# Optimization experiments

Hardware: AMD Instinct MI355X
Metric: run time of the kernel (lower is better)

The kernel has to match this reference:

```python
import jax, jax.numpy as jnp
import numpy as np

DIM = 1024
H = 8            # heads (light and heavy)
DH = 64          # dim_head
W = 64           # local attention window (light_window_size // 2)
NQ = 512         # num_heavy_tokens_q
NKV = 1024       # num_heavy_tokens_kv
EPS = 1.0        # coor descent eps
NITERS = 50      # coor descent iters
FETCH = 9.0 / 8.0
SCALE = DH ** -0.5


def _ln(x, w, b):
    m = x.mean(-1, keepdims=True)
    v = ((x - m) ** 2).mean(-1, keepdims=True)
    return (x - m) * jax.lax.rsqrt(v + 1e-5) * w + b


def _rms(x, g):
    n = jnp.maximum(jnp.linalg.norm(x, axis=-1, keepdims=True), 1e-12)
    return x / n * np.sqrt(DIM).astype(np.float32) * g


def local_attn(x, Wqkv, Wout):
    # LocalMHA, non-causal, look_backward=1, look_forward=1, window W
    b, n, _ = x.shape
    nw = n // W
    qkv = x @ Wqkv.T                      # [b,n,3*H*DH]
    q, k, v = jnp.split(qkv, 3, axis=-1)
    def towin(t):
        return t.reshape(b, nw, W, H, DH).transpose(0, 3, 1, 2, 4)  # [b,h,nw,w,dh]
    q, k, v = map(towin, (q, k, v))
    def expand(t):  # gather prev/cur/next windows -> [b,h,nw,3w,dh]
        tp = jnp.pad(t, ((0, 0), (0, 0), (1, 1), (0, 0), (0, 0)))
        return jnp.concatenate([tp[:, :, :-2], tp[:, :, 1:-1], tp[:, :, 2:]], axis=3)
    ke, ve = expand(k), expand(v)
    sim = jnp.einsum('bhnid,bhnjd->bhnij', q, ke) * SCALE
    win = jnp.arange(nw)
    valid = jnp.concatenate([
        jnp.repeat((win > 0)[:, None], W, 1),
        jnp.ones((nw, W), bool),
        jnp.repeat((win < nw - 1)[:, None], W, 1)], axis=1)  # [nw,3w]
    sim = jnp.where(valid[None, None, :, None, :], sim, -1e9)
    attn = jax.nn.softmax(sim, axis=-1)
    o = jnp.einsum('bhnij,bhnjd->bhnid', attn, ve)
    o = o.transpose(0, 2, 3, 1, 4).reshape(b, n, H * DH)
    return o @ Wout.T


def route(x, routing_token, num_tokens):
    # CoordinateDescentRouter with num_routing_tokens=1, straight_through=True
    s = jnp.einsum('bnd,rd->brn', x, routing_token).reshape(x.shape[0], x.shape[1])
    n = s.shape[-1]
    logk = jnp.log(jnp.asarray(min(num_tokens * FETCH, float(n)), s.dtype))
    def body(ab, _):
        a, bb = ab
        a = EPS * (logk - jax.nn.logsumexp((s + bb) / EPS, axis=-1, keepdims=True))
        bb = -jax.nn.relu(s + a)
        return (a, bb), None
    (a, bb), _ = jax.lax.scan(body, (jnp.zeros((s.shape[0], 1), s.dtype), -s), None, length=NITERS)
    scores = jnp.exp((s + a + bb) / EPS)
    sel_scores, sel_idx = jax.lax.top_k(scores, num_tokens)
    # straight-through: forward value 1.0, gradient of identity
    sel_scores = sel_scores + jax.lax.stop_gradient(1.0 - sel_scores)
    return sel_scores, sel_idx


def heavy_attn(xq, ctx, scores_kv, gamma, Wq, Wkv, Wout, null_kv):
    b = xq.shape[0]
    xq = _rms(xq, gamma)
    ctx = _rms(ctx, gamma)
    q = (xq @ Wq.T).reshape(b, -1, H, DH).transpose(0, 2, 1, 3)           # [b,h,nq,dh]
    kv = (ctx @ Wkv.T).reshape(b, -1, H, 2 * DH).transpose(0, 2, 1, 3)    # [b,h,nkv,2dh]
    k, v = kv[..., :DH], kv[..., DH:]
    v = v * scores_kv[:, None, :, None]
    nk = jnp.broadcast_to(null_kv[0][None, :, None, :], (b, H, 1, DH))
    nv = jnp.broadcast_to(null_kv[1][None, :, None, :], (b, H, 1, DH))
    k = jnp.concatenate([nk, k], axis=2)
    v = jnp.concatenate([nv, v], axis=2)
    sim = jnp.einsum('bhid,bhjd->bhij', q, k) * SCALE
    attn = jax.nn.softmax(sim, axis=-1)
    o = jnp.einsum('bhij,bhjd->bhid', attn, v)
    o = o.transpose(0, 2, 1, 3).reshape(b, -1, H * DH)
    return o @ Wout.T


def setup_inputs() -> dict:
    key = jax.random.key(0)
    ks = jax.random.split(key, 12)
    D, IN = DIM, H * DH
    w = lambda k, shape: jax.random.normal(k, shape, jnp.float32) * 0.02
    return {
        'x': jax.random.normal(ks[0], (4, 4096, D), jnp.float32),
        'ln_w': jnp.ones((D,), jnp.float32),
        'ln_b': jnp.zeros((D,), jnp.float32),
        'Wqkv': w(ks[1], (3 * IN, D)),
        'Wout_l': w(ks[2], (D, IN)),
        'rt_q': jax.random.normal(ks[3], (1, D), jnp.float32),
        'rt_kv': jax.random.normal(ks[4], (1, D), jnp.float32),
        'gamma': jnp.ones((D,), jnp.float32),
        'Wq': w(ks[5], (IN, D)),
        'Wkv': w(ks[6], (2 * IN, D)),
        'Wout_h': w(ks[7], (D, IN)),
        'null_kv': jax.random.normal(ks[8], (2, H, DH), jnp.float32),
        'null_q': jax.random.normal(ks[9], (D,), jnp.float32),
    }


def reference(x, ln_w, ln_b, Wqkv, Wout_l, rt_q, rt_kv, gamma, Wq, Wkv, Wout_h, null_kv, null_q):
    b, n, d = x.shape
    light = local_attn(_ln(x, ln_w, ln_b), Wqkv, Wout_l)
    sq, iq = route(x, rt_q, NQ)
    skv, ikv = route(x, rt_kv, NKV)
    br = jnp.arange(b)[:, None]
    xq = x[br, iq]          # gather routed queries  [b,NQ,d]
    xkv = x[br, ikv]        # gather routed kv       [b,NKV,d]
    heavy = heavy_attn(xq, xkv, skv, gamma, Wq, Wkv, Wout_h, null_kv)
    heavy = heavy * sq[..., None]
    out = jnp.broadcast_to(null_q[None, None, :], (b, n, d))
    out = out.at[br, iq].set(heavy)   # scatter heavy branch back
    return out + light
```

## Files before the change

### kernel.cpp

```cpp
#include <hip/hip_runtime.h>
#include <hip/hip_bf16.h>

typedef __attribute__((ext_vector_type(8))) short bv8;
typedef __attribute__((ext_vector_type(4))) float fv4;
typedef __hip_bfloat16 bf16;

#define MFMA16(a,b,c) __builtin_amdgcn_mfma_f32_16x16x32_bf16((a),(b),(c),0,0,0)
#define GLOAD_LDS(gp, lp) __builtin_amdgcn_global_load_lds( \
    (const __attribute__((address_space(1))) void*)(gp), \
    (__attribute__((address_space(3))) void*)(lp), 16, 0, 0)

template<int NW>
__device__ __forceinline__ float blockReduceSumF(float v) {
  #pragma unroll
  for (int m = 1; m < 64; m <<= 1) v += __shfl_xor(v, m, 64);
  __shared__ float sm[NW];
  if ((threadIdx.x & 63) == 0) sm[threadIdx.x >> 6] = v;
  __syncthreads();
  float t = 0.f;
  #pragma unroll
  for (int i = 0; i < NW; ++i) t += sm[i];
  __syncthreads();
  return t;
}

template<int NW>
__device__ __forceinline__ double blockReduceMaxD(double v) {
  #pragma unroll
  for (int m = 1; m < 64; m <<= 1) v = fmax(v, __shfl_xor(v, m, 64));
  __shared__ double sm[NW];
  if ((threadIdx.x & 63) == 0) sm[threadIdx.x >> 6] = v;
  __syncthreads();
  double t = sm[0];
  #pragma unroll
  for (int i = 1; i < NW; ++i) t = fmax(t, sm[i]);
  __syncthreads();
  return t;
}

__global__ __launch_bounds__(256)
void prep_kernel(const float* __restrict__ x, const float* __restrict__ lnw,
                 const float* __restrict__ lnb, const float* __restrict__ rtq,
                 const float* __restrict__ rtkv, bf16* __restrict__ lnout,
                 double* __restrict__ s,
                 const float* __restrict__ a0, const float* __restrict__ a1,
                 const float* __restrict__ a2, const float* __restrict__ a3,
                 const float* __restrict__ a4,
                 bf16* __restrict__ b0, bf16* __restrict__ b1, bf16* __restrict__ b2,
                 bf16* __restrict__ b3, bf16* __restrict__ b4,
                 int* __restrict__ posq) {
  const int bid = blockIdx.x;
  if (bid < 16384) {
    const int r = bid;
    const float* xr = x + (size_t)r * 1024;
    float v4[4]; float ssum = 0.f;
    double dq = 0.0, dk = 0.0;
    #pragma unroll
    for (int i = 0; i < 4; ++i) {
      int d = threadIdx.x + i * 256;
      float v = xr[d];
      v4[i] = v; ssum += v;
      dq += (double)v * (double)rtq[d];
      dk += (double)v * (double)rtkv[d];
    }
    ssum = blockReduceSumF<4>(ssum);
    const float mean = ssum * (1.0f / 1024.0f);
    float vs = 0.f;
    #pragma unroll
    for (int i = 0; i < 4; ++i) { float d = v4[i] - mean; vs += d * d; }
    vs = blockReduceSumF<4>(vs);
    const float rstd = 1.0f / sqrtf(vs * (1.0f / 1024.0f) + 1e-5f);
    #pragma unroll
    for (int m = 1; m < 64; m <<= 1) { dq += __shfl_xor(dq, m, 64); dk += __shfl_xor(dk, m, 64); }
    __shared__ double smq[4], smk[4];
    if ((threadIdx.x & 63) == 0) { smq[threadIdx.x >> 6] = dq; smk[threadIdx.x >> 6] = dk; }
    __syncthreads();
    if (threadIdx.x == 0) {
      s[r] = smq[0] + smq[1] + smq[2] + smq[3];
      s[16384 + r] = smk[0] + smk[1] + smk[2] + smk[3];
    }
    bf16* orow = lnout + (size_t)r * 1024;
    #pragma unroll
    for (int i = 0; i < 4; ++i) {
      int d = threadIdx.x + i * 256;
      orow[d] = __float2bfloat16((v4[i] - mean) * rstd * lnw[d] + lnb[d]);
    }
  } else if (bid < 18432) {
    size_t g = ((size_t)(bid - 16384) * 256 + threadIdx.x) * 8;
    const float* src; bf16* dst; size_t off;
    if (g < 1572864)      { src = a0; dst = b0; off = g; }
    else if (g < 2097152) { src = a1; dst = b1; off = g - 1572864; }
    else if (g < 2621440) { src = a2; dst = b2; off = g - 2097152; }
    else if (g < 3670016) { src = a3; dst = b3; off = g - 2621440; }
    else                  { src = a4; dst = b4; off = g - 3670016; }
    float4 v0 = *(const float4*)(src + off);
    float4 v1 = *(const float4*)(src + off + 4);
    bv8 o;
    ((bf16*)&o)[0] = __float2bfloat16(v0.x); ((bf16*)&o)[1] = __float2bfloat16(v0.y);
    ((bf16*)&o)[2] = __float2bfloat16(v0.z); ((bf16*)&o)[3] = __float2bfloat16(v0.w);
    ((bf16*)&o)[4] = __float2bfloat16(v1.x); ((bf16*)&o)[5] = __float2bfloat16(v1.y);
    ((bf16*)&o)[6] = __float2bfloat16(v1.z); ((bf16*)&o)[7] = __float2bfloat16(v1.w);
    *(bv8*)(dst + off) = o;
  } else {
    int i0 = (bid - 18432) * 1024 + threadIdx.x * 4;
    posq[i0] = -1; posq[i0 + 1] = -1; posq[i0 + 2] = -1; posq[i0 + 3] = -1;
  }
}

__global__ __launch_bounds__(256, 1)
void route_sel_kernel(const double* __restrict__ s_all, int* __restrict__ iq,
                      int* __restrict__ ikv, int* __restrict__ posq) {
  const int route = blockIdx.x >> 2, b = blockIdx.x & 3;
  const double* s = s_all + route * 16384 + b * 4096;
  const double K = (route == 0) ? 576.0 : 1152.0;
  const int KSEL = (route == 0) ? 512 : 1024;
  const int tid = threadIdx.x;
  const int lane = tid & 63, wid = tid >> 6;
  __shared__ double evbuf[4096];
  __shared__ double a_sh;
  __shared__ int scn[256];

  double sv[16];
  #pragma unroll
  for (int i = 0; i < 16; ++i) sv[i] = s[tid * 16 + i];
  double mx = sv[0];
  #pragma unroll
  for (int i = 1; i < 16; ++i) mx = fmax(mx, sv[i]);
  mx = blockReduceMaxD<4>(mx);
  #pragma unroll
  for (int i = 0; i < 16; ++i) evbuf[tid * 16 + i] = exp(sv[i] - mx);
  __syncthreads();

  if (wid == 0) {
    double e64[64];
    #pragma unroll
    for (int j = 0; j < 64; ++j) e64[j] = evbuf[j * 64 + lane];
    double z = (4096.0 / K) * exp(-mx);
    for (int it = 1; it < 50; ++it) {
      double a0 = 0.0, a1 = 0.0, a2 = 0.0, a3 = 0.0;
      #pragma unroll
      for (int j = 0; j < 64; j += 4) {
        a0 += fmin(e64[j], z);
        a1 += fmin(e64[j + 1], z);
        a2 += fmin(e64[j + 2], z);
        a3 += fmin(e64[j + 3], z);
      }
      double t = (a0 + a1) + (a2 + a3);
      #pragma unroll
      for (int m = 1; m < 64; m <<= 1) t += __shfl_xor(t, m, 64);
      z = t / K;
    }
    if (lane == 0) a_sh = -mx - log(z);
  }
  __syncthreads();
  const double a = a_sh;

  float scf[16]; int m16 = 0;
  #pragma unroll
  for (int i = 0; i < 16; ++i) {
    scf[i] = (float)exp(fmin(sv[i] + a, 0.0));
    m16 += (scf[i] == 1.0f) ? 1 : 0;
  }
  scn[tid] = m16;
  __syncthreads();
  for (int off = 1; off < 256; off <<= 1) {
    int v = (tid >= off) ? scn[tid - off] : 0;
    __syncthreads();
    scn[tid] += v;
    __syncthreads();
  }
  const int total = scn[255];
  const int excl = scn[tid] - m16;
  if (total >= KSEL) {
    int rk = excl;
    #pragma unroll
    for (int i = 0; i < 16; ++i) {
      if (scf[i] == 1.0f) {
        if (rk < KSEL) {
          int idx = tid * 16 + i;
          if (route == 0) { iq[b * 512 + rk] = idx; posq[b * 4096 + idx] = rk; }
          else            { ikv[b * 1024 + rk] = idx; }
        }
        rk++;
      }
    }
  } else {
    unsigned long long* keys = (unsigned long long*)evbuf;
    #pragma unroll
    for (int i = 0; i < 16; ++i) {
      unsigned bits = __float_as_uint(scf[i]);
      keys[tid * 16 + i] = ((unsigned long long)(~bits) << 32) | (unsigned long long)(tid * 16 + i);
    }
    for (int k = 2; k <= 4096; k <<= 1) {
      for (int j = k >> 1; j > 0; j >>= 1) {
        __syncthreads();
        for (int t = tid; t < 2048; t += 256) {
          int i2 = ((t & ~(j - 1)) << 1) | (t & (j - 1));
          int ip = i2 + j;
          unsigned long long av = keys[i2], bvv = keys[ip];
          bool up = ((i2 & k) == 0);
          if (up ? (av > bvv) : (av < bvv)) { keys[i2] = bvv; keys[ip] = av; }
        }
      }
    }
    __syncthreads();
    for (int j2 = tid; j2 < KSEL; j2 += 256) {
      int idx = (int)(keys[j2] & 0xFFFFFFFFull);
      if (route == 0) { iq[b * 512 + j2] = idx; posq[b * 4096 + idx] = j2; }
      else            { ikv[b * 1024 + j2] = idx; }
    }
  }
}

template<int EPI>
__device__ __forceinline__ void gemm_core(
    const bf16* __restrict__ A, const bf16* __restrict__ B, void* __restrict__ Cout,
    int N, int K, int row0, int col0, bf16* As, bf16* Bs,
    const int* __restrict__ posq, const float* __restrict__ heavy,
    const float* __restrict__ nullq) {
  const int tid = threadIdx.x;
  const int lane = tid & 63, w = tid >> 6;
  const int wr = w >> 1, wc = w & 1;
  const int lrow = lane & 15, lk = (lane >> 4) * 8;
  fv4 acc[4][4];
  #pragma unroll
  for (int m = 0; m < 4; ++m)
    #pragma unroll
    for (int n = 0; n < 4; ++n) acc[m][n] = (fv4){0.f, 0.f, 0.f, 0.f};
  const int ob0 = w * 2048;
  for (int k0 = 0; k0 < K; k0 += 32) {
    #pragma unroll
    for (int t = 0; t < 2; ++t) {
      int ob = ob0 + t * 1024;
      int ofl = ob + lane * 16;
      int r = ofl >> 6, c8 = ((ofl >> 4) & 3) * 8;
      GLOAD_LDS(A + (size_t)(row0 + r) * K + k0 + c8, (char*)As + ob);
      GLOAD_LDS(B + (size_t)(col0 + r) * K + k0 + c8, (char*)Bs + ob);
    }
    __syncthreads();
    bv8 af[4], bfr[4];
    #pragma unroll
    for (int m = 0; m < 4; ++m) af[m] = *(bv8*)&As[(wr * 64 + m * 16 + lrow) * 32 + lk];
    #pragma unroll
    for (int n = 0; n < 4; ++n) bfr[n] = *(bv8*)&Bs[(wc * 64 + n * 16 + lrow) * 32 + lk];
    #pragma unroll
    for (int m = 0; m < 4; ++m)
      #pragma unroll
      for (int n = 0; n < 4; ++n)
        acc[m][n] = MFMA16(af[m], bfr[n], acc[m][n]);
    __syncthreads();
  }
  #pragma unroll
  for (int m = 0; m < 4; ++m) {
    int gr0 = row0 + wr * 64 + m * 16 + (lane >> 4) * 4;
    #pragma unroll
    for (int n = 0; n < 4; ++n) {
      int gc = col0 + wc * 64 + n * 16 + lrow;
      #pragma unroll
      for (int r = 0; r < 4; ++r) {
        int grow = gr0 + r;
        float vv = acc[m][n][r];
        if (EPI == 0) {
          ((bf16*)Cout)[(size_t)grow * N + gc] = __float2bfloat16(vv);
        } else if (EPI == 1) {
          ((float*)Cout)[(size_t)grow * N + gc] = vv;
        } else {
          int p = posq[grow];
          float add = (p >= 0) ? heavy[((size_t)((grow >> 12) * 512 + p)) * 1024 + gc]
                               : nullq[gc];
          ((float*)Cout)[(size_t)grow * N + gc] = vv + add;
        }
      }
    }
  }
}

__device__ __forceinline__ void xcd_remap(int d, int gx, int& row0, int& col0) {
  int q = d >> 3;
  col0 = (q % gx) * 128;
  row0 = ((d & 7) + 8 * (q / gx)) * 128;
}

template<int EPI>
__global__ __launch_bounds__(256)
void gemm_bt(const bf16* __restrict__ A, const bf16* __restrict__ B, void* __restrict__ Cout,
             int N, int K,
             const int* __restrict__ posq, const float* __restrict__ heavy,
             const float* __restrict__ nullq) {
  __shared__ alignas(16) bf16 As[128 * 32];
  __shared__ alignas(16) bf16 Bs[128 * 32];
  int row0, col0;
  xcd_remap(blockIdx.y * gridDim.x + blockIdx.x, gridDim.x, row0, col0);
  gemm_core<EPI>(A, B, Cout, N, K, row0, col0, As, Bs, posq, heavy, nullq);
}

__global__ __launch_bounds__(256)
void wqkv_gemm_kernel(const bf16* __restrict__ xkv, const bf16* __restrict__ Wkv,
                      bf16* __restrict__ kvh,
                      const bf16* __restrict__ xq, const bf16* __restrict__ Wq,
                      bf16* __restrict__ qh) {
  __shared__ alignas(16) bf16 As[128 * 32];
  __shared__ alignas(16) bf16 Bs[128 * 32];
  const int bid = blockIdx.x;
  int row0, col0;
  if (bid < 256) {
    xcd_remap(bid, 8, row0, col0);
    gemm_core<0>(xkv, Wkv, kvh, 1024, 1024, row0, col0, As, Bs, nullptr, nullptr, nullptr);
  } else {
    xcd_remap(bid - 256, 4, row0, col0);
    gemm_core<0>(xq, Wq, qh, 512, 1024, row0, col0, As, Bs, nullptr, nullptr, nullptr);
  }
}

__global__ __launch_bounds__(256)
void la_gather_kernel(const bf16* __restrict__ qkv, bf16* __restrict__ olight,
                      const float* __restrict__ x, const float* __restrict__ gamma,
                      const int* __restrict__ iq, const int* __restrict__ ikv,
                      bf16* __restrict__ xq, bf16* __restrict__ xkv) {
  __shared__ bf16 Qs[64][72], Ks[64][72], Vts[64][72], Ps[64][72];
  const int tid = threadIdx.x;
  if (blockIdx.x < 2048) {
    const int w = blockIdx.x & 63, h = (blockIdx.x >> 6) & 7, b = blockIdx.x >> 9;
    const int lane = tid & 63, wv = tid >> 6;
    const int lrow = lane & 15, lkg = lane >> 4;
    {
      const size_t baseq = ((size_t)(b * 4096 + w * 64)) * 1536 + h * 64;
      #pragma unroll
      for (int v = 0; v < 2; ++v) {
        int vec = tid + v * 256; int i = vec >> 3, dd = (vec & 7) * 8;
        *(bv8*)&Qs[i][dd] = *(const bv8*)&qkv[baseq + (size_t)i * 1536 + dd];
      }
    }
    fv4 oacc[4];
    float m_run[4], l_run[4];
    #pragma unroll
    for (int n = 0; n < 4; ++n) oacc[n] = (fv4){0.f, 0.f, 0.f, 0.f};
    #pragma unroll
    for (int r = 0; r < 4; ++r) { m_run[r] = -INFINITY; l_run[r] = 0.f; }
    for (int c = 0; c < 3; ++c) {
      int sw = w - 1 + c;
      if (sw < 0 || sw >= 64) continue;
      __syncthreads();
      const size_t bkv = ((size_t)(b * 4096 + sw * 64)) * 1536 + h * 64;
      #pragma unroll
      for (int v = 0; v < 2; ++v) {
        int vec = tid + v * 256; int i = vec >> 3, dd = (vec & 7) * 8;
        *(bv8*)&Ks[i][dd] = *(const bv8*)&qkv[bkv + 512 + (size_t)i * 1536 + dd];
      }
      #pragma unroll
      for (int v = 0; v < 2; ++v) {
        int vec = tid + v * 256; int j = vec >> 3, d0 = (vec & 7) * 8;
        bv8 val = *(const bv8*)&qkv[bkv + 1024 + (size_t)j * 1536 + d0];
        #pragma unroll
        for (int i = 0; i < 8; ++i) Vts[d0 + i][j] = ((bf16*)&val)[i];
      }
      __syncthreads();
      fv4 sa[4];
      #pragma unroll
      for (int n = 0; n < 4; ++n) {
        sa[n] = (fv4){0.f, 0.f, 0.f, 0.f};
        #pragma unroll
        for (int ks = 0; ks < 2; ++ks) {
          bv8 aq = *(bv8*)&Qs[wv * 16 + lrow][lkg * 8 + ks * 32];
          bv8 bk = *(bv8*)&Ks[n * 16 + lrow][lkg * 8 + ks * 32];
          sa[n] = MFMA16(aq, bk, sa[n]);
        }
      }
      float mc[4];
      #pragma unroll
      for (int r = 0; r < 4; ++r) {
        #pragma unroll
        for (int n = 0; n < 4; ++n) sa[n][r] *= 0.125f;
        mc[r] = fmaxf(fmaxf(sa[0][r], sa[1][r]), fmaxf(sa[2][r], sa[3][r]));
      }
      #pragma unroll
      for (int m = 1; m < 16; m <<= 1)
        #pragma unroll
        for (int r = 0; r < 4; ++r) mc[r] = fmaxf(mc[r], __shfl_xor(mc[r], m, 64));
      float p[4][4], ls[4];
      #pragma unroll
      for (int r = 0; r < 4; ++r) {
        float mn = fmaxf(m_run[r], mc[r]);
        float scl = expf(m_run[r] - mn);
        ls[r] = 0.f;
        #pragma unroll
        for (int n = 0; n < 4; ++n) { p[n][r] = expf(sa[n][r] - mn); ls[r] += p[n][r]; }
        m_run[r] = mn;
        l_run[r] *= scl;
        #pragma unroll
        for (int n = 0; n < 4; ++n) oacc[n][r] *= scl;
      }
      #pragma unroll
      for (int m = 1; m < 16; m <<= 1)
        #pragma unroll
        for (int r = 0; r < 4; ++r) ls[r] += __shfl_xor(ls[r], m, 64);
      #pragma unroll
      for (int r = 0; r < 4; ++r) l_run[r] += ls[r];
      #pragma unroll
      for (int n = 0; n < 4; ++n)
        #pragma unroll
        for (int r = 0; r < 4; ++r)
          Ps[wv * 16 + lkg * 4 + r][n * 16 + lrow] = __float2bfloat16(p[n][r]);
      __syncthreads();
      #pragma unroll
      for (int n = 0; n < 4; ++n)
        #pragma unroll
        for (int ks = 0; ks < 2; ++ks) {
          bv8 ap = *(bv8*)&Ps[wv * 16 + lrow][lkg * 8 + ks * 32];
          bv8 bvv = *(bv8*)&Vts[n * 16 + lrow][lkg * 8 + ks * 32];
          oacc[n] = MFMA16(ap, bvv, oacc[n]);
        }
    }
    const size_t ob = ((size_t)(b * 4096 + w * 64 + wv * 16)) * 512 + h * 64;
    #pragma unroll
    for (int n = 0; n < 4; ++n)
      #pragma unroll
      for (int r = 0; r < 4; ++r) {
        int row = lkg * 4 + r;
        olight[ob + (size_t)row * 512 + n * 16 + lrow] = __float2bfloat16(oacc[n][r] / l_run[r]);
      }
  } else {
    const int bid = blockIdx.x - 2048;
    const float* src; bf16* dst;
    if (bid < 2048) {
      int b = bid >> 9, j = bid & 511;
      int tok = iq[b * 512 + j];
      src = x + ((size_t)(b * 4096 + tok)) * 1024;
      dst = xq + (size_t)bid * 1024;
    } else {
      int id = bid - 2048;
      int b = id >> 10, j = id & 1023;
      int tok = ikv[b * 1024 + j];
      src = x + ((size_t)(b * 4096 + tok)) * 1024;
      dst = xkv + (size_t)id * 1024;
    }
    float v4[4]; float ss = 0.f;
    #pragma unroll
    for (int i = 0; i < 4; ++i) { v4[i] = src[tid + i * 256]; ss += v4[i] * v4[i]; }
    ss = blockReduceSumF<4>(ss);
    const float nrm = fmaxf(sqrtf(ss), 1e-12f);
    const float scl = 32.0f / nrm;
    #pragma unroll
    for (int i = 0; i < 4; ++i) {
      int d = tid + i * 256;
      dst[d] = __float2bfloat16(v4[i] * scl * gamma[d]);
    }
  }
}

__global__ __launch_bounds__(256)
void heavy_attn_split_kernel(const bf16* __restrict__ qh, const bf16* __restrict__ kvh,
                             const float* __restrict__ nkv, bf16* __restrict__ o_part,
                             float* __restrict__ ml_part) {
  const int qt = blockIdx.x, h = blockIdx.y;
  const int b = blockIdx.z >> 2, s = blockIdx.z & 3;
  const int tid = threadIdx.x;
  const int lane = tid & 63, wv = tid >> 6;
  const int lrow = lane & 15, lkg = lane >> 4;
  __shared__ bf16 Qs[64][72], Ks[64][72], Vts[64][72], Ps[64][72];
  {
    const size_t baseq = ((size_t)(b * 512 + qt * 64)) * 512 + h * 64;
    #pragma unroll
    for (int v = 0; v < 2; ++v) {
      int vec = tid + v * 256; int i = vec >> 3, dd = (vec & 7) * 8;
      *(bv8*)&Qs[i][dd] = *(const bv8*)&qh[baseq + (size_t)i * 512 + dd];
    }
  }
  fv4 oacc[4];
  float m_run[4], l_run[4];
  #pragma unroll
  for (int n = 0; n < 4; ++n) oacc[n] = (fv4){0.f, 0.f, 0.f, 0.f};
  #pragma unroll
  for (int r = 0; r < 4; ++r) { m_run[r] = -INFINITY; l_run[r] = 0.f; }
  const int cs = (s == 0) ? 0 : (s * 4 + 1);
  const int ce = s * 4 + 5;
  for (int c = cs; c < ce; ++c) {
    __syncthreads();
    #pragma unroll
    for (int v = 0; v < 2; ++v) {
      int vec = tid + v * 256; int j = vec >> 3, dd = (vec & 7) * 8;
      int kvg = c * 64 + j;
      bv8 val;
      if (kvg >= 1 && kvg <= 1024) {
        val = *(const bv8*)&kvh[((size_t)(b * 1024 + kvg - 1)) * 1024 + h * 128 + dd];
      } else if (kvg == 0) {
        #pragma unroll
        for (int t = 0; t < 8; ++t) ((bf16*)&val)[t] = __float2bfloat16(nkv[h * 64 + dd + t]);
      } else {
        #pragma unroll
        for (int t = 0; t < 8; ++t) ((short*)&val)[t] = 0;
      }
      *(bv8*)&Ks[j][dd] = val;
    }
    #pragma unroll
    for (int v = 0; v < 2; ++v) {
      int vec = tid + v * 256; int j = vec >> 3, d0 = (vec & 7) * 8;
      int kvg = c * 64 + j;
      if (kvg >= 1 && kvg <= 1024) {
        bv8 val = *(const bv8*)&kvh[((size_t)(b * 1024 + kvg - 1)) * 1024 + h * 128 + 64 + d0];
        #pragma unroll
        for (int i = 0; i < 8; ++i) Vts[d0 + i][j] = ((bf16*)&val)[i];
      } else if (kvg == 0) {
        #pragma unroll
        for (int i = 0; i < 8; ++i) Vts[d0 + i][j] = __float2bfloat16(nkv[512 + h * 64 + d0 + i]);
      } else {
        #pragma unroll
        for (int i = 0; i < 8; ++i) Vts[d0 + i][j] = __float2bfloat16(0.0f);
      }
    }
    __syncthreads();
    fv4 sa[4];
    #pragma unroll
    for (int n = 0; n < 4; ++n) {
      sa[n] = (fv4){0.f, 0.f, 0.f, 0.f};
      #pragma unroll
      for (int ks = 0; ks < 2; ++ks) {
        bv8 aq = *(bv8*)&Qs[wv * 16 + lrow][lkg * 8 + ks * 32];
        bv8 bk = *(bv8*)&Ks[n * 16 + lrow][lkg * 8 + ks * 32];
        sa[n] = MFMA16(aq, bk, sa[n]);
      }
    }
    float mc[4];
    #pragma unroll
    for (int r = 0; r < 4; ++r) {
      #pragma unroll
      for (int n = 0; n < 4; ++n) {
        sa[n][r] *= 0.125f;
        int kvg = c * 64 + n * 16 + lrow;
        if (kvg > 1024) sa[n][r] = -1e30f;
      }
      mc[r] = fmaxf(fmaxf(sa[0][r], sa[1][r]), fmaxf(sa[2][r], sa[3][r]));
    }
    #pragma unroll
    for (int m = 1; m < 16; m <<= 1)
      #pragma unroll
      for (int r = 0; r < 4; ++r) mc[r] = fmaxf(mc[r], __shfl_xor(mc[r], m, 64));
    float p[4][4], ls[4];
    #pragma unroll
    for (int r = 0; r < 4; ++r) {
      float mn = fmaxf(m_run[r], mc[r]);
      float scl = expf(m_run[r] - mn);
      ls[r] = 0.f;
      #pragma unroll
      for (int n = 0; n < 4; ++n) { p[n][r] = expf(sa[n][r] - mn); ls[r] += p[n][r]; }
      m_run[r] = mn;
      l_run[r] *= scl;
      #pragma unroll
      for (int n = 0; n < 4; ++n) oacc[n][r] *= scl;
    }
    #pragma unroll
    for (int m = 1; m < 16; m <<= 1)
      #pragma unroll
      for (int r = 0; r < 4; ++r) ls[r] += __shfl_xor(ls[r], m, 64);
    #pragma unroll
    for (int r = 0; r < 4; ++r) l_run[r] += ls[r];
    #pragma unroll
    for (int n = 0; n < 4; ++n)
      #pragma unroll
      for (int r = 0; r < 4; ++r)
        Ps[wv * 16 + lkg * 4 + r][n * 16 + lrow] = __float2bfloat16(p[n][r]);
    __syncthreads();
    #pragma unroll
    for (int n = 0; n < 4; ++n)
      #pragma unroll
      for (int ks = 0; ks < 2; ++ks) {
        bv8 ap = *(bv8*)&Ps[wv * 16 + lrow][lkg * 8 + ks * 32];
        bv8 bvv = *(bv8*)&Vts[n * 16 + lrow][lkg * 8 + ks * 32];
        oacc[n] = MFMA16(ap, bvv, oacc[n]);
      }
  }
  const int idx = (((s * 4 + b) * 8 + h) * 8 + qt);
  bf16* ob = o_part + (size_t)idx * 4096;
  #pragma unroll
  for (int n = 0; n < 4; ++n)
    #pragma unroll
    for (int r = 0; r < 4; ++r) {
      int row = wv * 16 + lkg * 4 + r;
      ob[row * 64 + n * 16 + lrow] = __float2bfloat16(oacc[n][r]);
    }
  if (lrow == 0) {
    #pragma unroll
    for (int r = 0; r < 4; ++r) {
      int row = wv * 16 + lkg * 4 + r;
      ml_part[idx * 128 + row] = m_run[r];
      ml_part[idx * 128 + 64 + row] = l_run[r];
    }
  }
}

__global__ __launch_bounds__(256)
void heavy_combine_kernel(const bf16* __restrict__ o_part, const float* __restrict__ ml_part,
                          bf16* __restrict__ oh) {
  const int qt = blockIdx.x, h = blockIdx.y, b = blockIdx.z;
  const int tid = threadIdx.x;
  const int row = tid >> 2, c0 = (tid & 3) * 16;
  int idx[4]; float m[4], l[4];
  #pragma unroll
  for (int s = 0; s < 4; ++s) {
    idx[s] = (((s * 4 + b) * 8 + h) * 8 + qt);
    m[s] = ml_part[idx[s] * 128 + row];
    l[s] = ml_part[idx[s] * 128 + 64 + row];
  }
  const float mstar = fmaxf(fmaxf(m[0], m[1]), fmaxf(m[2], m[3]));
  float wsum = 0.f, w[4];
  #pragma unroll
  for (int s = 0; s < 4; ++s) { w[s] = expf(m[s] - mstar); wsum += w[s] * l[s]; }
  const float inv = 1.0f / wsum;
  float o[16];
  #pragma unroll
  for (int i = 0; i < 16; ++i) o[i] = 0.f;
  #pragma unroll
  for (int s = 0; s < 4; ++s) {
    const bf16* op = o_part + (size_t)idx[s] * 4096 + row * 64 + c0;
    bv8 v0 = *(const bv8*)op;
    bv8 v1 = *(const bv8*)(op + 8);
    #pragma unroll
    for (int j = 0; j < 8; ++j) o[j] += w[s] * __bfloat162float(((bf16*)&v0)[j]);
    #pragma unroll
    for (int j = 0; j < 8; ++j) o[8 + j] += w[s] * __bfloat162float(((bf16*)&v1)[j]);
  }
  const size_t ob = ((size_t)(b * 512 + qt * 64 + row)) * 512 + h * 64 + c0;
  bv8 pk[2];
  #pragma unroll
  for (int i = 0; i < 16; ++i) ((bf16*)pk)[i] = __float2bfloat16(o[i] * inv);
  *(bv8*)&oh[ob] = pk[0];
  *(bv8*)&oh[ob + 8] = pk[1];
}

extern "C" void kernel_launch(void* const* d_in, const int* in_sizes, int n_in,
                              void* d_out, int out_size, void* d_ws, size_t ws_size,
                              hipStream_t stream) {
  (void)in_sizes; (void)n_in; (void)out_size; (void)ws_size;
  const float* x     = (const float*)d_in[0];
  const float* ln_w  = (const float*)d_in[1];
  const float* ln_b  = (const float*)d_in[2];
  const float* Wqkv  = (const float*)d_in[3];
  const float* Woutl = (const float*)d_in[4];
  const float* rtq   = (const float*)d_in[5];
  const float* rtkv  = (const float*)d_in[6];
  const float* gamma = (const float*)d_in[7];
  const float* Wq    = (const float*)d_in[8];
  const float* Wkv   = (const float*)d_in[9];
  const float* Wouth = (const float*)d_in[10];
  const float* nkv   = (const float*)d_in[11];
  const float* nq    = (const float*)d_in[12];
  float* out = (float*)d_out;

  char* ws = (char*)d_ws;
  size_t off = 0;
  auto alloc = [&](size_t bytes) -> void* {
    void* p = ws + off;
    off = (off + bytes + 255) & ~(size_t)255;
    return p;
  };
  bf16* ln_bf    = (bf16*)alloc(16384ull * 1024 * 2);
  bf16* qkv_bf   = (bf16*)alloc(16384ull * 1536 * 2);
  bf16* ol_bf    = (bf16*)alloc(16384ull * 512 * 2);
  bf16* Wqkv_bf  = (bf16*)alloc(1536ull * 1024 * 2);
  bf16* Woutl_bf = (bf16*)alloc(1024ull * 512 * 2);
  bf16* Wq_bf    = (bf16*)alloc(512ull * 1024 * 2);
  bf16* Wkv_bf   = (bf16*)alloc(1024ull * 1024 * 2);
  bf16* Wouth_bf = (bf16*)alloc(1024ull * 512 * 2);
  double* s_d    = (double*)alloc(32768ull * 8);
  int* iq        = (int*)alloc(2048ull * 4);
  int* ikv       = (int*)alloc(4096ull * 4);
  int* posq      = (int*)alloc(16384ull * 4);
  bf16* xq_bf    = (bf16*)alloc(2048ull * 1024 * 2);
  bf16* xkv_bf   = (bf16*)alloc(4096ull * 1024 * 2);
  bf16* qh_bf    = (bf16*)alloc(2048ull * 512 * 2);
  bf16* kvh_bf   = (bf16*)alloc(4096ull * 1024 * 2);
  bf16* oh_bf    = (bf16*)alloc(2048ull * 512 * 2);
  float* heavy_f = (float*)alloc(2048ull * 1024 * 4);
  bf16* o_part   = (bf16*)alloc(4096ull * 4096 * 2);
  float* ml_part = (float*)alloc(4096ull * 128 * 4);

  prep_kernel<<<18448, 256, 0, stream>>>(x, ln_w, ln_b, rtq, rtkv, ln_bf, s_d,
                                         Wqkv, Woutl, Wq, Wkv, Wouth,
                                         Wqkv_bf, Woutl_bf, Wq_bf, Wkv_bf, Wouth_bf,
                                         posq);

  route_sel_kernel<<<8, 256, 0, stream>>>(s_d, iq, ikv, posq);

  gemm_bt<0><<<dim3(12, 128), 256, 0, stream>>>(ln_bf, Wqkv_bf, qkv_bf, 1536, 1024,
                                                nullptr, nullptr, nullptr);

  la_gather_kernel<<<8192, 256, 0, stream>>>(qkv_bf, ol_bf, x, gamma, iq, ikv, xq_bf, xkv_bf);

  wqkv_gemm_kernel<<<320, 256, 0, stream>>>(xkv_bf, Wkv_bf, kvh_bf, xq_bf, Wq_bf, qh_bf);

  heavy_attn_split_kernel<<<dim3(8, 8, 16), 256, 0, stream>>>(qh_bf, kvh_bf, nkv, o_part, ml_part);
  heavy_combine_kernel<<<dim3(8, 8, 4), 256, 0, stream>>>(o_part, ml_part, oh_bf);
  gemm_bt<1><<<dim3(8, 16), 256, 0, stream>>>(oh_bf, Wouth_bf, heavy_f, 1024, 512,
                                              nullptr, nullptr, nullptr);

  gemm_bt<2><<<dim3(8, 128), 256, 0, stream>>>(ol_bf, Woutl_bf, out, 1024, 512,
                                               posq, heavy_f, nq);
}
```

Before: 293.7 us.

## Regroup kernels: co-launch independent stages and fuse heavy combine into Wout GEMM

The big QKV GEMM now shares a launch with the routed-token gather/RMS-norm. Light local attention shares a launch with the heavy Q/KV projection GEMM, so independent work runs side by side in one grid. The split-KV combine of heavy attention is folded into the A-operand load of the heavy output GEMM, which removes a kernel launch and the oh intermediate buffer. In exchange, each GEMM block recomputes the combine weights, and the A-tile load becomes a synchronous register path instead of direct global-to-LDS loads.

Measured after the change: 287.1 us. -2.2%, faster.

```diff
diff --git a/kernel.cpp b/kernel.cpp
--- a/kernel.cpp
+++ b/kernel.cpp
@@ -295,34 +295,78 @@
 }
 
 __global__ __launch_bounds__(256)
-void wqkv_gemm_kernel(const bf16* __restrict__ xkv, const bf16* __restrict__ Wkv,
-                      bf16* __restrict__ kvh,
-                      const bf16* __restrict__ xq, const bf16* __restrict__ Wq,
-                      bf16* __restrict__ qh) {
-  __shared__ alignas(16) bf16 As[128 * 32];
-  __shared__ alignas(16) bf16 Bs[128 * 32];
+void qkv_gather_kernel(const bf16* __restrict__ ln, const bf16* __restrict__ Wqkv,
+                       bf16* __restrict__ qkv,
+                       const float* __restrict__ x, const float* __restrict__ gamma,
+                       const int* __restrict__ iq, const int* __restrict__ ikv,
+                       bf16* __restrict__ xq, bf16* __restrict__ xkv) {
   const int bid = blockIdx.x;
-  int row0, col0;
-  if (bid < 256) {
-    xcd_remap(bid, 8, row0, col0);
-    gemm_core<0>(xkv, Wkv, kvh, 1024, 1024, row0, col0, As, Bs, nullptr, nullptr, nullptr);
+  const int tid = threadIdx.x;
+  if (bid < 1536) {
+    __shared__ alignas(16) bf16 As[128 * 32];
+    __shared__ alignas(16) bf16 Bs[128 * 32];
+    int row0, col0;
+    xcd_remap(bid, 12, row0, col0);
+    gemm_core<0>(ln, Wqkv, qkv, 1536, 1024, row0, col0, As, Bs, nullptr, nullptr, nullptr);
   } else {
-    xcd_remap(bid - 256, 4, row0, col0);
-    gemm_core<0>(xq, Wq, qh, 512, 1024, row0, col0, As, Bs, nullptr, nullptr, nullptr);
+    const int gid = bid - 1536;
+    const float* src; bf16* dst;
+    if (gid < 2048) {
+      int b = gid >> 9, j = gid & 511;
+      int tok = iq[b * 512 + j];
+      src = x + ((size_t)(b * 4096 + tok)) * 1024;
+      dst = xq + (size_t)gid * 1024;
+    } else {
+      int id = gid - 2048;
+      int b = id >> 10, j = id & 1023;
+      int tok = ikv[b * 1024 + j];
+      src = x + ((size_t)(b * 4096 + tok)) * 1024;
+      dst = xkv + (size_t)id * 1024;
+    }
+    float v4[4]; float ss = 0.f;
+    #pragma unroll
+    for (int i = 0; i < 4; ++i) { v4[i] = src[tid + i * 256]; ss += v4[i] * v4[i]; }
+    ss = blockReduceSumF<4>(ss);
+    const float nrm = fmaxf(sqrtf(ss), 1e-12f);
+    const float scl = 32.0f / nrm;
+    #pragma unroll
+    for (int i = 0; i < 4; ++i) {
+      int d = tid + i * 256;
+      dst[d] = __float2bfloat16(v4[i] * scl * gamma[d]);
+    }
   }
 }
 
 __global__ __launch_bounds__(256)
-void la_gather_kernel(const bf16* __restrict__ qkv, bf16* __restrict__ olight,
-                      const float* __restrict__ x, const float* __restrict__ gamma,
-                      const int* __restrict__ iq, const int* __restrict__ ikv,
-                      bf16* __restrict__ xq, bf16* __restrict__ xkv) {
-  __shared__ bf16 Qs[64][72], Ks[64][72], Vts[64][72], Ps[64][72];
+void la_wqkv_kernel(const bf16* __restrict__ qkv, bf16* __restrict__ olight,
+                    const bf16* __restrict__ xkv, const bf16* __restrict__ Wkv,
+                    bf16* __restrict__ kvh,
+                    const bf16* __restrict__ xq, const bf16* __restrict__ Wq,
+                    bf16* __restrict__ qh) {
+  __shared__ __align__(16) char smem_raw[36864];
   const int tid = threadIdx.x;
-  if (blockIdx.x < 2048) {
-    const int w = blockIdx.x & 63, h = (blockIdx.x >> 6) & 7, b = blockIdx.x >> 9;
+  const int bid = blockIdx.x;
+  if (bid < 320) {
+    bf16* As = (bf16*)smem_raw;
+    bf16* Bs = (bf16*)(smem_raw + 8192);
+    int row0, col0;
+    if (bid < 256) {
+      xcd_remap(bid, 8, row0, col0);
+      gemm_core<0>(xkv, Wkv, kvh, 1024, 1024, row0, col0, As, Bs, nullptr, nullptr, nullptr);
+    } else {
+      xcd_remap(bid - 256, 4, row0, col0);
+      gemm_core<0>(xq, Wq, qh, 512, 1024, row0, col0, As, Bs, nullptr, nullptr, nullptr);
+    }
+  } else {
+    const int lid = bid - 320;
+    const int w = lid & 63, h = (lid >> 6) & 7, b = lid >> 9;
     const int lane = tid & 63, wv = tid >> 6;
     const int lrow = lane & 15, lkg = lane >> 4;
+    typedef bf16 row72[72];
+    row72* Qs  = (row72*)smem_raw;
+    row72* Ks  = (row72*)(smem_raw + 9216);
+    row72* Vts = (row72*)(smem_raw + 18432);
+    row72* Ps  = (row72*)(smem_raw + 27648);
     {
       const size_t baseq = ((size_t)(b * 4096 + w * 64)) * 1536 + h * 64;
       #pragma unroll
@@ -419,32 +463,6 @@
         int row = lkg * 4 + r;
         olight[ob + (size_t)row * 512 + n * 16 + lrow] = __float2bfloat16(oacc[n][r] / l_run[r]);
       }
-  } else {
-    const int bid = blockIdx.x - 2048;
-    const float* src; bf16* dst;
-    if (bid < 2048) {
-      int b = bid >> 9, j = bid & 511;
-      int tok = iq[b * 512 + j];
-      src = x + ((size_t)(b * 4096 + tok)) * 1024;
-      dst = xq + (size_t)bid * 1024;
-    } else {
-      int id = bid - 2048;
-      int b = id >> 10, j = id & 1023;
-      int tok = ikv[b * 1024 + j];
-      src = x + ((size_t)(b * 4096 + tok)) * 1024;
-      dst = xkv + (size_t)id * 1024;
-    }
-    float v4[4]; float ss = 0.f;
-    #pragma unroll
-    for (int i = 0; i < 4; ++i) { v4[i] = src[tid + i * 256]; ss += v4[i] * v4[i]; }
-    ss = blockReduceSumF<4>(ss);
-    const float nrm = fmaxf(sqrtf(ss), 1e-12f);
-    const float scl = 32.0f / nrm;
-    #pragma unroll
-    for (int i = 0; i < 4; ++i) {
-      int d = tid + i * 256;
-      dst[d] = __float2bfloat16(v4[i] * scl * gamma[d]);
-    }
   }
 }
 
@@ -589,42 +607,81 @@
 }
 
 __global__ __launch_bounds__(256)
-void heavy_combine_kernel(const bf16* __restrict__ o_part, const float* __restrict__ ml_part,
-                          bf16* __restrict__ oh) {
-  const int qt = blockIdx.x, h = blockIdx.y, b = blockIdx.z;
+void wouth_gemm_kernel(const bf16* __restrict__ o_part, const float* __restrict__ ml_part,
+                       const bf16* __restrict__ B, float* __restrict__ Cout) {
+  __shared__ alignas(16) bf16 As[128 * 32];
+  __shared__ alignas(16) bf16 Bs[128 * 32];
+  const int N = 1024, K = 512;
+  int row0, col0;
+  xcd_remap(blockIdx.y * gridDim.x + blockIdx.x, gridDim.x, row0, col0);
   const int tid = threadIdx.x;
-  const int row = tid >> 2, c0 = (tid & 3) * 16;
-  int idx[4]; float m[4], l[4];
-  #pragma unroll
-  for (int s = 0; s < 4; ++s) {
-    idx[s] = (((s * 4 + b) * 8 + h) * 8 + qt);
-    m[s] = ml_part[idx[s] * 128 + row];
-    l[s] = ml_part[idx[s] * 128 + 64 + row];
-  }
-  const float mstar = fmaxf(fmaxf(m[0], m[1]), fmaxf(m[2], m[3]));
-  float wsum = 0.f, w[4];
-  #pragma unroll
-  for (int s = 0; s < 4; ++s) { w[s] = expf(m[s] - mstar); wsum += w[s] * l[s]; }
-  const float inv = 1.0f / wsum;
-  float o[16];
-  #pragma unroll
-  for (int i = 0; i < 16; ++i) o[i] = 0.f;
-  #pragma unroll
-  for (int s = 0; s < 4; ++s) {
-    const bf16* op = o_part + (size_t)idx[s] * 4096 + row * 64 + c0;
-    bv8 v0 = *(const bv8*)op;
-    bv8 v1 = *(const bv8*)(op + 8);
-    #pragma unroll
-    for (int j = 0; j < 8; ++j) o[j] += w[s] * __bfloat162float(((bf16*)&v0)[j]);
-    #pragma unroll
-    for (int j = 0; j < 8; ++j) o[8 + j] += w[s] * __bfloat162float(((bf16*)&v1)[j]);
-  }
-  const size_t ob = ((size_t)(b * 512 + qt * 64 + row)) * 512 + h * 64 + c0;
-  bv8 pk[2];
-  #pragma unroll
-  for (int i = 0; i < 16; ++i) ((bf16*)pk)[i] = __float2bfloat16(o[i] * inv);
-  *(bv8*)&oh[ob] = pk[0];
-  *(bv8*)&oh[ob + 8] = pk[1];
+  const int lane = tid & 63, w = tid >> 6;
+  const int wr = w >> 1, wc = w & 1;
+  const int lrow = lane & 15, lk = (lane >> 4) * 8;
+  fv4 acc[4][4];
+  #pragma unroll
+  for (int m = 0; m < 4; ++m)
+    #pragma unroll
+    for (int n = 0; n < 4; ++n) acc[m][n] = (fv4){0.f, 0.f, 0.f, 0.f};
+  const int ob0 = w * 2048;
+  for (int k0 = 0; k0 < K; k0 += 32) {
+    #pragma unroll
+    for (int t = 0; t < 2; ++t) {
+      int ob = ob0 + t * 1024;
+      int ofl = ob + lane * 16;
+      int r = ofl >> 6, c8 = ((ofl >> 4) & 3) * 8;
+      int grow = row0 + r, k = k0 + c8;
+      int b = grow >> 9, qrow = grow & 511;
+      int qt = qrow >> 6, row_in = qrow & 63;
+      int h = k >> 6, d0 = k & 63;
+      bv8 v[4]; float m[4], l[4];
+      #pragma unroll
+      for (int s = 0; s < 4; ++s) {
+        int idx = (((s * 4 + b) * 8 + h) * 8 + qt);
+        v[s] = *(const bv8*)&o_part[(size_t)idx * 4096 + row_in * 64 + d0];
+        m[s] = ml_part[idx * 128 + row_in];
+        l[s] = ml_part[idx * 128 + 64 + row_in];
+      }
+      float mstar = fmaxf(fmaxf(m[0], m[1]), fmaxf(m[2], m[3]));
+      float ws[4]; float wsum = 0.f;
+      #pragma unroll
+      for (int s = 0; s < 4; ++s) { ws[s] = expf(m[s] - mstar); wsum += ws[s] * l[s]; }
+      const float inv = 1.0f / wsum;
+      bv8 o8;
+      #pragma unroll
+      for (int j = 0; j < 8; ++j) {
+        float acc8 = 0.f;
+        #pragma unroll
+        for (int s = 0; s < 4; ++s) acc8 += ws[s] * __bfloat162float(((bf16*)&v[s])[j]);
+        ((bf16*)&o8)[j] = __float2bfloat16(acc8 * inv);
+      }
+      *(bv8*)((char*)As + ofl) = o8;
+      GLOAD_LDS(B + (size_t)(col0 + r) * K + k0 + c8, (char*)Bs + ob);
+    }
+    __syncthreads();
+    bv8 af[4], bfr[4];
+    #pragma unroll
+    for (int m2 = 0; m2 < 4; ++m2) af[m2] = *(bv8*)&As[(wr * 64 + m2 * 16 + lrow) * 32 + lk];
+    #pragma unroll
+    for (int n = 0; n < 4; ++n) bfr[n] = *(bv8*)&Bs[(wc * 64 + n * 16 + lrow) * 32 + lk];
+    #pragma unroll
+    for (int m2 = 0; m2 < 4; ++m2)
+      #pragma unroll
+      for (int n = 0; n < 4; ++n)
+        acc[m2][n] = MFMA16(af[m2], bfr[n], acc[m2][n]);
+    __syncthreads();
+  }
+  #pragma unroll
+  for (int m2 = 0; m2 < 4; ++m2) {
+    int gr0 = row0 + wr * 64 + m2 * 16 + (lane >> 4) * 4;
+    #pragma unroll
+    for (int n = 0; n < 4; ++n) {
+      int gc = col0 + wc * 64 + n * 16 + lrow;
+      #pragma unroll
+      for (int r = 0; r < 4; ++r)
+        Cout[(size_t)(gr0 + r) * N + gc] = acc[m2][n][r];
+    }
+  }
 }
 
 extern "C" void kernel_launch(void* const* d_in, const int* in_sizes, int n_in,
@@ -669,7 +726,6 @@
   bf16* xkv_bf   = (bf16*)alloc(4096ull * 1024 * 2);
   bf16* qh_bf    = (bf16*)alloc(2048ull * 512 * 2);
   bf16* kvh_bf   = (bf16*)alloc(4096ull * 1024 * 2);
-  bf16* oh_bf    = (bf16*)alloc(2048ull * 512 * 2);
   float* heavy_f = (float*)alloc(2048ull * 1024 * 4);
   bf16* o_part   = (bf16*)alloc(4096ull * 4096 * 2);
   float* ml_part = (float*)alloc(4096ull * 128 * 4);
@@ -681,17 +737,16 @@
 
   route_sel_kernel<<<8, 256, 0, stream>>>(s_d, iq, ikv, posq);
 
-  gemm_bt<0><<<dim3(12, 128), 256, 0, stream>>>(ln_bf, Wqkv_bf, qkv_bf, 1536, 1024,
-                                                nullptr, nullptr, nullptr);
-
-  la_gather_kernel<<<8192, 256, 0, stream>>>(qkv_bf, ol_bf, x, gamma, iq, ikv, xq_bf, xkv_bf);
-
-  wqkv_gemm_kernel<<<320, 256, 0, stream>>>(xkv_bf, Wkv_bf, kvh_bf, xq_bf, Wq_bf, qh_bf);
+  qkv_gather_kernel<<<7680, 256, 0, stream>>>(ln_bf, Wqkv_bf, qkv_bf,
+                                              x, gamma, iq, ikv, xq_bf, xkv_bf);
+
+  la_wqkv_kernel<<<2368, 256, 0, stream>>>(qkv_bf, ol_bf,
+                                           xkv_bf, Wkv_bf, kvh_bf,
+                                           xq_bf, Wq_bf, qh_bf);
 
   heavy_attn_split_kernel<<<dim3(8, 8, 16), 256, 0, stream>>>(qh_bf, kvh_bf, nkv, o_part, ml_part);
-  heavy_combine_kernel<<<dim3(8, 8, 4), 256, 0, stream>>>(o_part, ml_part, oh_bf);
-  gemm_bt<1><<<dim3(8, 16), 256, 0, stream>>>(oh_bf, Wouth_bf, heavy_f, 1024, 512,
-                                              nullptr, nullptr, nullptr);
+
+  wouth_gemm_kernel<<<dim3(8, 16), 256, 0, stream>>>(o_part, ml_part, Wouth_bf, heavy_f);
 
   gemm_bt<2><<<dim3(8, 128), 256, 0, stream>>>(ol_bf, Woutl_bf, out, 1024, 512,
                                                posq, heavy_f, nq);
```
